# Kernel tuning notes

Hardware: AMD Instinct MI355X
Metric: run time of the kernel (lower is better)

Reference implementation:

```python
import jax, jax.numpy as jnp
import numpy as np

H = 4      # heads
D = 32     # per-head / input channel dim
B, N = 1, 256


def setup_inputs() -> dict:
    key = jax.random.key(0)
    ks = jax.random.split(key, 10)
    x = jax.random.normal(ks[0], (B, N, N, D), dtype=jnp.float32)
    # binary key mask (1 = keep, 0 = masked out)
    mask = (jax.random.uniform(ks[1], (B, N, N)) > 0.15).astype(jnp.float32)
    s = 1.0 / np.sqrt(D)
    Wq = jax.random.normal(ks[2], (H * D, D), dtype=jnp.float32) * s
    bq = jnp.zeros((H * D,), dtype=jnp.float32)
    Wk = jax.random.normal(ks[3], (H * D, D), dtype=jnp.float32) * s
    bk = jnp.zeros((H * D,), dtype=jnp.float32)
    Wv = jax.random.normal(ks[4], (H * D, D), dtype=jnp.float32) * s
    bv = jnp.zeros((H * D,), dtype=jnp.float32)
    Wb = jax.random.normal(ks[5], (H, D), dtype=jnp.float32) * s
    bb = jnp.zeros((H,), dtype=jnp.float32)
    return {"x": x, "mask": mask, "Wq": Wq, "bq": bq, "Wk": Wk, "bk": bk,
            "Wv": Wv, "bv": bv, "Wb": Wb, "bb": bb}


def reference(x, mask, Wq, bq, Wk, bk, Wv, bv, Wb, bb):
    b_, i_, j_, d_ = x.shape
    # QKV projections -> [B, I, J, H, D]
    q = (x @ Wq.T + bq).reshape(b_, i_, j_, H, d_)
    k = (x @ Wk.T + bk).reshape(b_, i_, j_, H, d_)
    v = (x @ Wv.T + bv).reshape(b_, i_, j_, H, d_)
    # pairwise triangle bias: [B, I, J, H] -> [B, H, J, K]
    tri_b = jnp.transpose(x @ Wb.T + bb, (0, 3, 1, 2))
    scale = 1.0 / jnp.sqrt(jnp.asarray(d_, x.dtype))
    # scores over the key index k along the row: [B, H, I, J, K]
    scores = jnp.einsum('bijhd,bikhd->bhijk', q, k) * scale
    scores = scores + tri_b[:, :, None, :, :]                 # triangle bias
    scores = scores + (mask - 1.0)[:, None, :, None, :] * 1e9  # key mask
    attn = jax.nn.softmax(scores, axis=-1)
    out = jnp.einsum('bhijk,bikhd->bijhd', attn, v)  # [B, I, J, H, D]
    return out
```

## Files before the change

### kernel.cpp

```cpp
#include <hip/hip_runtime.h>

#define HEADS 4
#define NN 256
#define DW 32
#define LOG2E 1.4426950408889634f

typedef __bf16 bf16x8 __attribute__((ext_vector_type(8)));
typedef float f32x4 __attribute__((ext_vector_type(4)));
typedef float f32x16 __attribute__((ext_vector_type(16)));
typedef unsigned int u32x4 __attribute__((ext_vector_type(4)));
typedef unsigned short ushort4v __attribute__((ext_vector_type(4)));

static __device__ __forceinline__ ushort f2bf(float f) {
  __bf16 h = (__bf16)f;
  ushort r;
  __builtin_memcpy(&r, &h, 2);
  return r;
}

static __device__ __forceinline__ unsigned cvt_pk_bf16(float lo, float hi) {
  unsigned r;
  asm("v_cvt_pk_bf16_f32 %0, %1, %2" : "=v"(r) : "v"(lo), "v"(hi));
  return r;
}

__global__ __launch_bounds__(256) void bias_kernel(
    const float* __restrict__ x, const float* __restrict__ Wb,
    const float* __restrict__ bb, float* __restrict__ bias_tl) {
  const int jt = blockIdx.x;
  const int h = blockIdx.y;
  const int k = threadIdx.x;
  const int kb = k >> 5;
  const int c = k & 31;
  const int hi = (c >> 2) & 1;
  const int r = (c & 3) + 4 * (c >> 3);
  float wb[DW];
#pragma unroll
  for (int d = 0; d < DW; ++d) wb[d] = Wb[h * DW + d];
  const float bbv = bb[h];
  float* dst = bias_tl + (((h * 8 + kb) * 2 + hi) * NN + jt * 8) * 16 + r;
#pragma unroll
  for (int jj = 0; jj < 8; ++jj) {
    const float* xr = x + ((jt * 8 + jj) * NN + k) * DW;
    float a0 = 0.f, a1 = 0.f;
#pragma unroll
    for (int cc = 0; cc < 8; ++cc) {
      const float4 v = reinterpret_cast<const float4*>(xr)[cc];
      a0 += v.x * wb[cc * 4 + 0] + v.z * wb[cc * 4 + 2];
      a1 += v.y * wb[cc * 4 + 1] + v.w * wb[cc * 4 + 3];
    }
    dst[jj * 16] = (a0 + a1 + bbv) * LOG2E;
  }
}

__global__ __launch_bounds__(256, 3) void attn_mfma(
    const float* __restrict__ x, const float* __restrict__ mask,
    const float* __restrict__ Wq, const float* __restrict__ bq,
    const float* __restrict__ Wk, const float* __restrict__ bk,
    const float* __restrict__ Wv, const float* __restrict__ bv,
    const float* __restrict__ bias_tl, float* __restrict__ out) {
  __shared__ __align__(16) ushort Kq[NN][40];
  __shared__ __align__(16) ushort Vt[DW][264];
  __shared__ __align__(16) float mk[NN];
  __shared__ __align__(16) float Ls[NN];

  const int bid = blockIdx.x;
  const int i = bid >> 2;
  const int h = bid & 3;
  const int t = threadIdx.x;
  const int w = t >> 6;
  const int l = t & 63;
  const int lo5 = l & 31;
  const int hi = l >> 5;
  const int lr = l & 15;
  const int lq = l >> 4;
  const int rowbase = w * 64;
  const float scale = 0.17677669529663687f * LOG2E;

  bf16x8 wqf[2], wkf[2], wvf[2];
#pragma unroll
  for (int nt = 0; nt < 2; ++nt) {
    const int dd = nt * 16 + lr;
    const float* rq = Wq + (h * DW + dd) * DW + lq * 8;
    const float* rk = Wk + (h * DW + dd) * DW + lq * 8;
    const float* rv = Wv + (h * DW + dd) * DW + lq * 8;
#pragma unroll
    for (int jj = 0; jj < 8; ++jj) {
      wqf[nt][jj] = (__bf16)rq[jj];
      wkf[nt][jj] = (__bf16)rk[jj];
      wvf[nt][jj] = (__bf16)rv[jj];
    }
  }

  bf16x8 af[4];
#pragma unroll
  for (int rt = 0; rt < 4; ++rt) {
    const float* xr = x + (i * NN + rowbase + rt * 16 + lr) * DW + lq * 8;
#pragma unroll
    for (int jj = 0; jj < 8; ++jj) af[rt][jj] = (__bf16)xr[jj];
  }

#pragma unroll
  for (int rt = 0; rt < 4; ++rt) {
#pragma unroll
    for (int nt = 0; nt < 2; ++nt) {
      const int dd = nt * 16 + lr;
      f32x4 z = {0.f, 0.f, 0.f, 0.f};
      f32x4 cq = __builtin_amdgcn_mfma_f32_16x16x32_bf16(af[rt], wqf[nt], z, 0, 0, 0);
      const float bqv = bq[h * DW + dd];
#pragma unroll
      for (int j = 0; j < 4; ++j)
        Kq[rowbase + rt * 16 + lq * 4 + j][dd] = f2bf((cq[j] + bqv) * scale);
    }
  }
  bf16x8 qb[2][2];
#pragma unroll
  for (int qt = 0; qt < 2; ++qt)
#pragma unroll
    for (int dh = 0; dh < 2; ++dh)
      qb[qt][dh] = *(const bf16x8*)&Kq[rowbase + qt * 32 + lo5][dh * 16 + 8 * hi];

#pragma unroll
  for (int rt = 0; rt < 4; ++rt) {
#pragma unroll
    for (int nt = 0; nt < 2; ++nt) {
      const int dd = nt * 16 + lr;
      f32x4 z = {0.f, 0.f, 0.f, 0.f};
      f32x4 ck = __builtin_amdgcn_mfma_f32_16x16x32_bf16(af[rt], wkf[nt], z, 0, 0, 0);
      f32x4 cv = __builtin_amdgcn_mfma_f32_16x16x32_bf16(af[rt], wvf[nt], z, 0, 0, 0);
      const float bkv = bk[h * DW + dd];
      const float bvv = bv[h * DW + dd];
#pragma unroll
      for (int j = 0; j < 4; ++j)
        Kq[rowbase + rt * 16 + lq * 4 + j][dd] = f2bf(ck[j] + bkv);
      ushort4v v4;
#pragma unroll
      for (int j = 0; j < 4; ++j) v4[j] = f2bf(cv[j] + bvv);
      *(ushort4v*)&Vt[dd][rowbase + rt * 16 + lq * 4] = v4;
    }
  }
  mk[t] = mask[i * NN + t];
  __syncthreads();

  f32x16 ot[2];
  float lsum[2] = {0.f, 0.f};
#pragma unroll
  for (int qt = 0; qt < 2; ++qt)
#pragma unroll
    for (int r = 0; r < 16; ++r) ot[qt][r] = 0.f;

  const float* btl = bias_tl + ((h * 8) * 2 + hi) * (NN * 16);

  f32x4 bc[4], bn[4];
  {
    const float* p = btl + (rowbase + lo5) * 16;
#pragma unroll
    for (int g = 0; g < 4; ++g) bc[g] = *(const f32x4*)(p + g * 4);
  }

  bf16x8 ka0, ka1, va0, va1;
  float4 mvv[4];

#pragma unroll 1
  for (int kb = 0; kb < 8; ++kb) {
    const int kbase = kb * 32;
    ka0 = *(const bf16x8*)&Kq[kbase + lo5][8 * hi];
    ka1 = *(const bf16x8*)&Kq[kbase + lo5][16 + 8 * hi];
    va0 = *(const bf16x8*)&Vt[lo5][kbase + 8 * hi];
    va1 = *(const bf16x8*)&Vt[lo5][kbase + 16 + 8 * hi];
#pragma unroll
    for (int g = 0; g < 4; ++g)
      mvv[g] = *(const float4*)&mk[kbase + 4 * hi + 8 * g];

    auto tile = [&](const int qt, const f32x4 bcur[4]) {
      f32x16 cc;
#pragma unroll
      for (int g = 0; g < 4; ++g)
#pragma unroll
        for (int e = 0; e < 4; ++e) cc[g * 4 + e] = bcur[g][e];
      __builtin_amdgcn_s_setprio(1);
      f32x16 st = __builtin_amdgcn_mfma_f32_32x32x16_bf16(ka0, qb[qt][0], cc, 0, 0, 0);
      st = __builtin_amdgcn_mfma_f32_32x32x16_bf16(ka1, qb[qt][1], st, 0, 0, 0);
      __builtin_amdgcn_s_setprio(0);

#pragma unroll
      for (int r = 0; r < 16; ++r)
        st[r] = __builtin_amdgcn_exp2f(st[r]) * (&mvv[r >> 2].x)[r & 3];
      float s0 = (st[0] + st[1]) + (st[2] + st[3]);
      float s1 = (st[4] + st[5]) + (st[6] + st[7]);
      float s2 = (st[8] + st[9]) + (st[10] + st[11]);
      float s3 = (st[12] + st[13]) + (st[14] + st[15]);
      lsum[qt] += (s0 + s1) + (s2 + s3);

#pragma unroll
      for (int half = 0; half < 2; ++half) {
        const int b0 = half * 8;
        unsigned w0, w1, w2, w3;
        {
          unsigned A = cvt_pk_bf16(st[b0 + 0], st[b0 + 1]);
          unsigned B = cvt_pk_bf16(st[b0 + 4], st[b0 + 5]);
          asm volatile("v_permlane32_swap_b32 %0, %1" : "+v"(A), "+v"(B));
          w0 = A; w2 = B;
        }
        {
          unsigned A = cvt_pk_bf16(st[b0 + 2], st[b0 + 3]);
          unsigned B = cvt_pk_bf16(st[b0 + 6], st[b0 + 7]);
          asm volatile("v_permlane32_swap_b32 %0, %1" : "+v"(A), "+v"(B));
          w1 = A; w3 = B;
        }
        u32x4 words = {w0, w1, w2, w3};
        const bf16x8 pf = __builtin_bit_cast(bf16x8, words);
        __builtin_amdgcn_s_setprio(1);
        ot[qt] = __builtin_amdgcn_mfma_f32_32x32x16_bf16(
            pf, half ? va1 : va0, ot[qt], 0, 0, 0);
        __builtin_amdgcn_s_setprio(0);
      }
    };

    {
      const float* p = btl + (kb * 2) * (NN * 16) + (rowbase + 32 + lo5) * 16;
#pragma unroll
      for (int g = 0; g < 4; ++g) bn[g] = *(const f32x4*)(p + g * 4);
      tile(0, bc);
#pragma unroll
      for (int g = 0; g < 4; ++g) bc[g] = bn[g];
    }
    {
      const int kbn = (kb + 1) & 7;
      const float* p = btl + (kbn * 2) * (NN * 16) + (rowbase + lo5) * 16;
#pragma unroll
      for (int g = 0; g < 4; ++g) bn[g] = *(const f32x4*)(p + g * 4);
      tile(1, bc);
#pragma unroll
      for (int g = 0; g < 4; ++g) bc[g] = bn[g];
    }
  }

#pragma unroll
  for (int qt = 0; qt < 2; ++qt) {
    const float ls = lsum[qt] + __shfl_xor(lsum[qt], 32);
    Ls[rowbase + qt * 32 + lo5] = 1.0f / ls;
  }

#pragma unroll
  for (int qt = 0; qt < 2; ++qt)
#pragma unroll
    for (int r = 0; r < 16; ++r) {
      const int qp = (r & 3) + 8 * (r >> 2) + 4 * hi;
      const int qrow = rowbase + qt * 32 + qp;
      out[((i * NN + qrow) * HEADS + h) * DW + lo5] = ot[qt][r] * Ls[qrow];
    }
}

extern "C" void kernel_launch(void* const* d_in, const int* in_sizes, int n_in,
                              void* d_out, int out_size, void* d_ws,
                              size_t ws_size, hipStream_t stream) {
  const float* x    = (const float*)d_in[0];
  const float* mask = (const float*)d_in[1];
  const float* Wq   = (const float*)d_in[2];
  const float* bq   = (const float*)d_in[3];
  const float* Wk   = (const float*)d_in[4];
  const float* bk   = (const float*)d_in[5];
  const float* Wv   = (const float*)d_in[6];
  const float* bv   = (const float*)d_in[7];
  const float* Wb   = (const float*)d_in[8];
  const float* bb   = (const float*)d_in[9];
  float* out = (float*)d_out;
  float* bias_tl = (float*)d_ws;

  bias_kernel<<<dim3(32, HEADS), 256, 0, stream>>>(x, Wb, bb, bias_tl);
  attn_mfma<<<NN * HEADS, 256, 0, stream>>>(x, mask, Wq, bq, Wk, bk, Wv, bv,
                                            bias_tl, out);
}
```

Measured before the change: 121.5 us.

## Restage bias kernel via LDS, compute all heads per block, relayout bias buffer

The bias kernel now runs one block per row q, stages that row of x into padded LDS with coalesced float4 loads, and computes all four heads from one register copy of x instead of re-reading x once per head. The bias workspace layout changes so that each store writes contiguous 4-float groups per q, and the attention kernel's bias loads are re-addressed to the new layout with a stride between groups. The aim is to cut redundant global reads of x and improve coalescing in the small bias kernel, at the cost of a more strided bias gather inside the main attention loop.

```diff
diff --git a/kernel.cpp b/kernel.cpp
--- a/kernel.cpp
+++ b/kernel.cpp
@@ -26,30 +26,47 @@
 
 __global__ __launch_bounds__(256) void bias_kernel(
     const float* __restrict__ x, const float* __restrict__ Wb,
-    const float* __restrict__ bb, float* __restrict__ bias_tl) {
-  const int jt = blockIdx.x;
-  const int h = blockIdx.y;
-  const int k = threadIdx.x;
-  const int kb = k >> 5;
-  const int c = k & 31;
-  const int hi = (c >> 2) & 1;
-  const int r = (c & 3) + 4 * (c >> 3);
-  float wb[DW];
-#pragma unroll
-  for (int d = 0; d < DW; ++d) wb[d] = Wb[h * DW + d];
-  const float bbv = bb[h];
-  float* dst = bias_tl + (((h * 8 + kb) * 2 + hi) * NN + jt * 8) * 16 + r;
-#pragma unroll
-  for (int jj = 0; jj < 8; ++jj) {
-    const float* xr = x + ((jt * 8 + jj) * NN + k) * DW;
+    const float* __restrict__ bb, float* __restrict__ bias2) {
+  __shared__ float xs[NN * 36];
+
+  const int q = blockIdx.x;
+  const int t = threadIdx.x;
+
+  const float* xr = x + q * (NN * DW);
+#pragma unroll
+  for (int cc = 0; cc < 8; ++cc) {
+    const int f = (cc * 256 + t) * 4;
+    const float4 v = *reinterpret_cast<const float4*>(xr + f);
+    const int k = f >> 5;
+    const int d = f & 31;
+    *reinterpret_cast<float4*>(&xs[k * 36 + d]) = v;
+  }
+  __syncthreads();
+
+  float xv[DW];
+#pragma unroll
+  for (int c = 0; c < 8; ++c) {
+    const float4 v = *reinterpret_cast<const float4*>(&xs[t * 36 + c * 4]);
+    xv[c * 4 + 0] = v.x; xv[c * 4 + 1] = v.y;
+    xv[c * 4 + 2] = v.z; xv[c * 4 + 3] = v.w;
+  }
+
+  const int kb = t >> 5;
+  const int c2 = t & 31;
+  const int e = c2 & 3;
+  const int hi = (c2 >> 2) & 1;
+  const int g = c2 >> 3;
+
+#pragma unroll
+  for (int h = 0; h < HEADS; ++h) {
     float a0 = 0.f, a1 = 0.f;
 #pragma unroll
-    for (int cc = 0; cc < 8; ++cc) {
-      const float4 v = reinterpret_cast<const float4*>(xr)[cc];
-      a0 += v.x * wb[cc * 4 + 0] + v.z * wb[cc * 4 + 2];
-      a1 += v.y * wb[cc * 4 + 1] + v.w * wb[cc * 4 + 3];
-    }
-    dst[jj * 16] = (a0 + a1 + bbv) * LOG2E;
+    for (int d = 0; d < DW; d += 2) {
+      a0 += xv[d] * Wb[h * DW + d];
+      a1 += xv[d + 1] * Wb[h * DW + d + 1];
+    }
+    bias2[((((h * 8 + kb) * 4 + g) * 2 + hi) * NN + q) * 4 + e] =
+        (a0 + a1 + bb[h]) * LOG2E;
   }
 }
 
@@ -58,7 +75,7 @@
     const float* __restrict__ Wq, const float* __restrict__ bq,
     const float* __restrict__ Wk, const float* __restrict__ bk,
     const float* __restrict__ Wv, const float* __restrict__ bv,
-    const float* __restrict__ bias_tl, float* __restrict__ out) {
+    const float* __restrict__ bias2, float* __restrict__ out) {
   __shared__ __align__(16) ushort Kq[NN][40];
   __shared__ __align__(16) ushort Vt[DW][264];
   __shared__ __align__(16) float mk[NN];
@@ -149,13 +166,13 @@
 #pragma unroll
     for (int r = 0; r < 16; ++r) ot[qt][r] = 0.f;
 
-  const float* btl = bias_tl + ((h * 8) * 2 + hi) * (NN * 16);
+  const float* btl = bias2 + h * (8 * 4 * 2 * NN * 4) + hi * (NN * 4);
 
   f32x4 bc[4], bn[4];
   {
-    const float* p = btl + (rowbase + lo5) * 16;
-#pragma unroll
-    for (int g = 0; g < 4; ++g) bc[g] = *(const f32x4*)(p + g * 4);
+    const float* p = btl + (rowbase + lo5) * 4;
+#pragma unroll
+    for (int g = 0; g < 4; ++g) bc[g] = *(const f32x4*)(p + g * (2 * NN * 4));
   }
 
   bf16x8 ka0, ka1, va0, va1;
@@ -218,18 +235,18 @@
     };
 
     {
-      const float* p = btl + (kb * 2) * (NN * 16) + (rowbase + 32 + lo5) * 16;
-#pragma unroll
-      for (int g = 0; g < 4; ++g) bn[g] = *(const f32x4*)(p + g * 4);
+      const float* p = btl + kb * (8 * NN * 4) + (rowbase + 32 + lo5) * 4;
+#pragma unroll
+      for (int g = 0; g < 4; ++g) bn[g] = *(const f32x4*)(p + g * (2 * NN * 4));
       tile(0, bc);
 #pragma unroll
       for (int g = 0; g < 4; ++g) bc[g] = bn[g];
     }
     {
       const int kbn = (kb + 1) & 7;
-      const float* p = btl + (kbn * 2) * (NN * 16) + (rowbase + lo5) * 16;
-#pragma unroll
-      for (int g = 0; g < 4; ++g) bn[g] = *(const f32x4*)(p + g * 4);
+      const float* p = btl + kbn * (8 * NN * 4) + (rowbase + lo5) * 4;
+#pragma unroll
+      for (int g = 0; g < 4; ++g) bn[g] = *(const f32x4*)(p + g * (2 * NN * 4));
       tile(1, bc);
 #pragma unroll
       for (int g = 0; g < 4; ++g) bc[g] = bn[g];
@@ -266,9 +283,9 @@
   const float* Wb   = (const float*)d_in[8];
   const float* bb   = (const float*)d_in[9];
   float* out = (float*)d_out;
-  float* bias_tl = (float*)d_ws;
-
-  bias_kernel<<<dim3(32, HEADS), 256, 0, stream>>>(x, Wb, bb, bias_tl);
+  float* bias2 = (float*)d_ws;
+
+  bias_kernel<<<NN, 256, 0, stream>>>(x, Wb, bb, bias2);
   attn_mfma<<<NN * HEADS, 256, 0, stream>>>(x, mask, Wq, bq, Wk, bk, Wv, bv,
-                                            bias_tl, out);
-}
+                                            bias2, out);
+}
```

Result: faster. 113.5 us (-6.6%).
